# Performance work log

Hardware: AMD Instinct MI355X
Metric: run time of the kernel (lower is better)

## Reference

```python
import jax, jax.numpy as jnp
import numpy as np

CHUNK_SIZE = 64      # rows per quantization chunk
EMBED_DIM = 1024
BLOCKSIZE = 4096     # bnb quantize_blockwise default
VOCAB = 128000


def setup_inputs() -> dict:
    key = jax.random.key(0)
    k1, k2, k3, k4 = jax.random.split(key, 4)
    n_chunks = VOCAB // CHUNK_SIZE                      # 2000
    blocks_per_chunk = (CHUNK_SIZE * EMBED_DIM) // BLOCKSIZE  # 16
    x = jax.random.randint(k1, (8, 4096), 0, VOCAB, dtype=jnp.int32)
    # 8-bit code indices into the 256-entry codebook
    q_idx = jax.random.randint(k2, (n_chunks, CHUNK_SIZE, EMBED_DIM), 0, 256, dtype=jnp.int32)
    # per-block absmax scales (positive)
    absmax = jax.random.uniform(k3, (n_chunks, blocks_per_chunk), dtype=jnp.float32, minval=0.01, maxval=1.0)
    # codebook (bnb dynamic map is a fixed sorted table in [-1,1]; random sorted stand-in)
    code = jnp.sort(jnp.tanh(jax.random.normal(k4, (256,), dtype=jnp.float32)))
    return {"x": x, "q_idx": q_idx, "absmax": absmax, "code": code}


def reference(x, q_idx, absmax, code):
    # Fused dequant-on-gather: only dequantize the indexed rows.
    # Equivalent math to: per chunk, dequantize_blockwise(q_w, state) = code[q_w] * absmax[flat//BLOCKSIZE]
    # then gather rows by (x - chunk_start).
    chunk = x // CHUNK_SIZE          # [B,S] which chunk each id lives in
    local = x % CHUNK_SIZE           # [B,S] row within the chunk
    q = q_idx[chunk, local]          # [B,S,D] code indices for the needed rows
    vals = code[q]                   # [B,S,D] dequantized unit values
    # block index within the chunk for each element of the row
    d = jnp.arange(EMBED_DIM, dtype=jnp.int32)
    blk = (local[..., None] * EMBED_DIM + d) // BLOCKSIZE  # [B,S,D]
    scale = absmax[chunk[..., None], blk]                   # [B,S,D]
    return vals * scale
```

## Files before the change

### kernel.cpp

```cpp
#include <hip/hip_runtime.h>


#define EMBED_DIM 1024

__global__ __launch_bounds__(256) void bnb8_embed_kernel(
    const int*   __restrict__ x,
    const int*   __restrict__ q_idx,
    const float* __restrict__ absmax,
    const float* __restrict__ code,
    float*       __restrict__ out)
{
    __shared__ float code_lds[256];
    const int tid = threadIdx.x;
    code_lds[tid] = code[tid];

    const int token = blockIdx.x;
    const int xv    = x[token];
    const int local = xv & 63;
    const int chunk = xv >> 6;
    const float scale = absmax[chunk * 16 + (local >> 2)];
    __syncthreads();

    const int4 q = ((const int4*)(q_idx + (size_t)xv * EMBED_DIM))[tid];
    float4 v;
    v.x = code_lds[q.x] * scale;
    v.y = code_lds[q.y] * scale;
    v.z = code_lds[q.z] * scale;
    v.w = code_lds[q.w] * scale;
    ((float4*)(out + (size_t)token * EMBED_DIM))[tid] = v;
}

extern "C" void kernel_launch(void* const* d_in, const int* in_sizes, int n_in,
                              void* d_out, int out_size, void* d_ws, size_t ws_size,
                              hipStream_t stream) {
    const int*   x      = (const int*)d_in[0];
    const int*   q_idx  = (const int*)d_in[1];
    const float* absmax = (const float*)d_in[2];
    const float* code   = (const float*)d_in[3];
    float*       out    = (float*)d_out;

    const int n_tokens = in_sizes[0];
    bnb8_embed_kernel<<<n_tokens, 256, 0, stream>>>(x, q_idx, absmax, code, out);
}
```

Baseline: 630.9 us.

## Use persistent grid-stride blocks with software-pipelined row prefetch and nontemporal stores

Launches a fixed grid of 2048 blocks that loop over tokens with a grid stride. Each iteration prefetches the next token's code-index row and scale and the token id after that, so loads overlap the current dequantize-and-store. Output is written with nontemporal stores to avoid polluting cache. This amortizes the codebook LDS load and block launch cost, at the price of fewer independent blocks in flight for latency hiding.

```diff
diff --git a/kernel.cpp b/kernel.cpp
--- a/kernel.cpp
+++ b/kernel.cpp
@@ -2,32 +2,58 @@
 
 
 #define EMBED_DIM 1024
+
+typedef float f32x4 __attribute__((ext_vector_type(4)));
+typedef int   i32x4 __attribute__((ext_vector_type(4)));
 
 __global__ __launch_bounds__(256) void bnb8_embed_kernel(
     const int*   __restrict__ x,
     const int*   __restrict__ q_idx,
     const float* __restrict__ absmax,
     const float* __restrict__ code,
-    float*       __restrict__ out)
+    float*       __restrict__ out,
+    int n_tokens)
 {
     __shared__ float code_lds[256];
     const int tid = threadIdx.x;
     code_lds[tid] = code[tid];
-
-    const int token = blockIdx.x;
-    const int xv    = x[token];
-    const int local = xv & 63;
-    const int chunk = xv >> 6;
-    const float scale = absmax[chunk * 16 + (local >> 2)];
     __syncthreads();
 
-    const int4 q = ((const int4*)(q_idx + (size_t)xv * EMBED_DIM))[tid];
-    float4 v;
-    v.x = code_lds[q.x] * scale;
-    v.y = code_lds[q.y] * scale;
-    v.z = code_lds[q.z] * scale;
-    v.w = code_lds[q.w] * scale;
-    ((float4*)(out + (size_t)token * EMBED_DIM))[tid] = v;
+    const int stride = gridDim.x;
+    const int t0 = blockIdx.x;
+    if (t0 >= n_tokens) return;
+
+    int  xv0 = x[t0];
+    const int t1 = t0 + stride;
+    int  xv1 = (t1 < n_tokens) ? x[t1] : 0;
+
+    i32x4 q0 = ((const i32x4*)(q_idx + (size_t)xv0 * EMBED_DIM))[tid];
+    float s0 = absmax[xv0 >> 2];
+
+    for (int t = t0; t < n_tokens; ) {
+        const int tn  = t + stride;
+        const int tnn = tn + stride;
+
+        i32x4 q1 = (i32x4)(0);
+        float s1 = 0.0f;
+        if (tn < n_tokens) {
+            q1 = ((const i32x4*)(q_idx + (size_t)xv1 * EMBED_DIM))[tid];
+            s1 = absmax[xv1 >> 2];
+        }
+        const int xv2 = (tnn < n_tokens) ? x[tnn] : 0;
+
+        f32x4 v;
+        v.x = code_lds[q0.x] * s0;
+        v.y = code_lds[q0.y] * s0;
+        v.z = code_lds[q0.z] * s0;
+        v.w = code_lds[q0.w] * s0;
+        __builtin_nontemporal_store(v, (f32x4*)(out + (size_t)t * EMBED_DIM) + tid);
+
+        t   = tn;
+        q0  = q1;
+        s0  = s1;
+        xv1 = xv2;
+    }
 }
 
 extern "C" void kernel_launch(void* const* d_in, const int* in_sizes, int n_in,
@@ -40,5 +66,7 @@
     float*       out    = (float*)d_out;
 
     const int n_tokens = in_sizes[0];
-    bnb8_embed_kernel<<<n_tokens, 256, 0, stream>>>(x, q_idx, absmax, code, out);
+    int grid = 2048;
+    if (grid > n_tokens) grid = n_tokens;
+    bnb8_embed_kernel<<<grid, 256, 0, stream>>>(x, q_idx, absmax, code, out, n_tokens);
 }
```

New measurement: 629.8 us. About the same (-0.2%).
